# Kernel optimization log

Measured on AMD Instinct MI355X. Metric: run time of the kernel, lower is better.

The kernel has to match this reference:

```python
import jax, jax.numpy as jnp
import numpy as np

NUM_HEADS = 12
NUM_LANDMARKS = 64
EPS_REG = 1e-4


def setup_inputs() -> dict:
    key = jax.random.key(0)
    k1, k2, k3 = jax.random.split(key, 3)
    B, N, C = 4, 4096, 768
    x = jax.random.normal(k1, (B, N, C), dtype=jnp.float32)
    w_qkv = jax.random.normal(k2, (3 * C, C), dtype=jnp.float32) * (C ** -0.5)
    w_proj = jax.random.normal(k3, (C, C), dtype=jnp.float32) * (C ** -0.5)
    b_proj = jnp.zeros((C,), dtype=jnp.float32)
    return {"x": x, "w_qkv": w_qkv, "w_proj": w_proj, "b_proj": b_proj}


def _landmark_pool(t, m):
    # t: [B, H, N, D]; assumes N % m == 0 (true for chosen shapes)
    B, H, N, D = t.shape
    seg = N // m
    return t.reshape(B, H, m, seg, D).mean(axis=3)


def reference(x, w_qkv, w_proj, b_proj):
    B, N, C = x.shape
    H = NUM_HEADS
    D = C // H
    m = min(NUM_LANDMARKS, N)
    scale = D ** -0.5

    qkv = x @ w_qkv.T                              # [B, N, 3C]
    qkv = qkv.reshape(B, N, 3, H, D).transpose(2, 0, 3, 1, 4)
    q, k, v = qkv[0], qkv[1], qkv[2]               # [B, H, N, D]

    q_lm = _landmark_pool(q, m)                    # [B, H, m, D]
    k_lm = _landmark_pool(k, m)                    # [B, H, m, D]

    attn_q_km = jax.nn.softmax(jnp.einsum('bhnd,bhmd->bhnm', q, k_lm) * scale, axis=-1)
    attn_qm_km = jax.nn.softmax(jnp.einsum('bhld,bhmd->bhlm', q_lm, k_lm) * scale, axis=-1)
    attn_qm_k = jax.nn.softmax(jnp.einsum('bhmd,bhnd->bhmn', q_lm, k) * scale, axis=-1)

    eye = jnp.eye(m, dtype=attn_qm_km.dtype)
    inv_mid = jnp.linalg.inv(attn_qm_km + EPS_REG * eye)   # [B, H, m, m]

    out = attn_q_km @ (inv_mid @ (attn_qm_k @ v))          # [B, H, N, D]
    out = out.transpose(0, 2, 1, 3).reshape(B, N, C)
    out = out @ w_proj.T + b_proj
    return out
```

## Files before the change

kernel.cpp:

```cpp
#include <hip/hip_runtime.h>

typedef unsigned short u16;
typedef __attribute__((ext_vector_type(8))) short bf16x8;
typedef __attribute__((ext_vector_type(8))) unsigned short u16x8;
typedef __attribute__((ext_vector_type(4))) unsigned short u16x4;
typedef __attribute__((ext_vector_type(4))) float f32x4;

#define NB 4
#define NH 12
#define NSEQ 4096
#define NC 768
#define ND 64
#define NM 64
#define NBH 48

__device__ __forceinline__ float b2f(u16 u){ unsigned v = ((unsigned)u)<<16; return __builtin_bit_cast(float, v); }
__device__ __forceinline__ u16 f2b(float f){ unsigned u = __builtin_bit_cast(unsigned, f); u = u + 0x7FFFu + ((u>>16)&1u); return (u16)(u>>16); }
__device__ __forceinline__ void split2(float f, u16& h, u16& l){
  h = f2b(f);
  l = f2b(f - b2f(h));
}

typedef const __attribute__((address_space(1))) unsigned int guint;
typedef __attribute__((address_space(3))) unsigned int luint;
__device__ __forceinline__ void gload16(const void* g, void* l){
  __builtin_amdgcn_global_load_lds((guint*)g, (luint*)l, 16, 0, 0);
}

__device__ __forceinline__ f32x4 mfma16x16(bf16x8 a, bf16x8 b, f32x4 c){
  return __builtin_amdgcn_mfma_f32_16x16x32_bf16(a, b, c, 0, 0, 0);
}

#define NX4 3145728
#define NWQ4 442368
#define NWP4 147456
__global__ __launch_bounds__(256) void k_split3(const float* __restrict__ x, const float* __restrict__ wq,
                                                const float* __restrict__ wp,
                                                u16* __restrict__ xh, u16* __restrict__ xl,
                                                u16* __restrict__ wqh, u16* __restrict__ wql,
                                                u16* __restrict__ wph, u16* __restrict__ wpl){
  int i = blockIdx.x*256 + threadIdx.x;
  const float* src; u16 *dh, *dl; int j;
  if (i < NX4){ src = x; dh = xh; dl = xl; j = i; }
  else if (i < NX4+NWQ4){ src = wq; dh = wqh; dl = wql; j = i - NX4; }
  else if (i < NX4+NWQ4+NWP4){ src = wp; dh = wph; dl = wpl; j = i - NX4 - NWQ4; }
  else return;
  f32x4 v = ((const f32x4*)src)[j];
  u16x4 hh, ll;
  #pragma unroll
  for (int e=0;e<4;++e){ u16 hb, lb; split2(v[e], hb, lb); hh[e]=hb; ll[e]=lb; }
  ((u16x4*)dh)[j] = hh; ((u16x4*)dl)[j] = ll;
}


__global__ __launch_bounds__(256) void k_qkv(const u16* __restrict__ xh, const u16* __restrict__ xl,
                                             const u16* __restrict__ wh, const u16* __restrict__ wl,
                                             u16* __restrict__ qh, u16* __restrict__ ql,
                                             u16* __restrict__ kh, u16* __restrict__ kl,
                                             u16* __restrict__ vTh, u16* __restrict__ vTl,
                                             float* __restrict__ qlmf, float* __restrict__ klmf,
                                             u16* __restrict__ qlmh, u16* __restrict__ qlml,
                                             u16* __restrict__ klmh, u16* __restrict__ klml){
  __shared__ u16 lds[32768];
  const int K = NC;
  int tid = threadIdx.x, wave = tid>>6, lane = tid&63;
  int wm = wave>>1, wn = wave&1;
  int bid = blockIdx.x;
  int swz = (bid&7)*288 + (bid>>3);
  int bx = swz % 18, by = swz / 18;
  int m0 = by*128, n0 = bx*128;
  int srow = lane>>3;
  int scol = ((lane&7) ^ srow)*8;
  const u16* src0; u16* dst0;
  if (wave==0){ src0 = xh + (size_t)m0*K; dst0 = lds; }
  else if (wave==1){ src0 = xl + (size_t)m0*K; dst0 = lds+8192; }
  else if (wave==2){ src0 = wh + (size_t)n0*K; dst0 = lds+16384; }
  else            { src0 = wl + (size_t)n0*K; dst0 = lds+24576; }
  f32x4 acc[4][4] = {};
  for (int k0=0; k0<K; k0+=64){
    #pragma unroll
    for (int it=0; it<16; ++it){
      int r = it*8;
      gload16(&src0[(size_t)(r+srow)*K + k0 + scol], &dst0[r*64]);
    }
    __syncthreads();
    #pragma unroll
    for (int kk=0; kk<2; ++kk){
      int sl = ((kk*4 + (lane>>4)) ^ (lane&7))*8;
      bf16x8 a_h[4], a_l[4], b_h[4], b_l[4];
      #pragma unroll
      for (int i=0;i<4;++i){
        int ro = (wm*64+i*16+(lane&15))*64 + sl;
        a_h[i] = *(const bf16x8*)&lds[ro]; a_l[i] = *(const bf16x8*)&lds[8192+ro];
      }
      #pragma unroll
      for (int j=0;j<4;++j){
        int ro = (wn*64+j*16+(lane&15))*64 + sl;
        b_h[j] = *(const bf16x8*)&lds[16384+ro]; b_l[j] = *(const bf16x8*)&lds[24576+ro];
      }
      #pragma unroll
      for (int i=0;i<4;++i)
        #pragma unroll
        for (int j=0;j<4;++j){
          acc[i][j] = mfma16x16(a_h[i], b_h[j], acc[i][j]);
          acc[i][j] = mfma16x16(a_h[i], b_l[j], acc[i][j]);
          acc[i][j] = mfma16x16(a_l[i], b_h[j], acc[i][j]);
        }
    }
    __syncthreads();
  }
  int rb = (lane>>4)*4, cb = lane&15;
  int b_ = m0>>12, nlo = m0&4095;
  if (n0 < 1536){
    int s = n0/768;
    u16* dh = s ? kh : qh;
    u16* dl = s ? kl : ql;
    float* lmf = s ? klmf : qlmf;
    u16* lmh = s ? klmh : qlmh;
    u16* lml = s ? klml : qlml;
    #pragma unroll
    for (int j=0;j<4;++j){
      int gn = n0 + wn*64 + j*16 + cb;
      int rem = gn - s*768; int hd = rem>>6, d = rem&63;
      #pragma unroll
      for (int i=0;i<4;++i)
        #pragma unroll
        for (int r=0;r<4;++r){
          int n = nlo + wm*64 + i*16 + rb + r;
          size_t idx = (((size_t)(b_*NH + hd))*NSEQ + n)*ND + d;
          u16 hb, lb; split2(acc[i][j][r], hb, lb);
          dh[idx] = hb; dl[idx] = lb;
        }
      float tot = 0.f;
      #pragma unroll
      for (int i=0;i<4;++i)
        #pragma unroll
        for (int r=0;r<4;++r) tot += acc[i][j][r];
      tot += __shfl_xor(tot, 16);
      tot += __shfl_xor(tot, 32);
      if (lane < 16){
        int lseg = (nlo>>6) + wm;
        float mean = tot * (1.f/64.f);
        size_t o = (((size_t)(b_*NH + hd))*NM + lseg)*ND + d;
        lmf[o] = mean;
        u16 hb, lb; split2(mean, hb, lb);
        lmh[o] = hb; lml[o] = lb;
      }
    }
  } else {
    const int TS = 136;
    #pragma unroll
    for (int part=0; part<2; ++part){
      __syncthreads();
      #pragma unroll
      for (int j=0;j<4;++j){
        int dcol = wn*64 + j*16 + cb;
        #pragma unroll
        for (int i=0;i<4;++i)
          #pragma unroll
          for (int r=0;r<4;++r){
            int nrow = wm*64 + i*16 + rb + r;
            u16 hb, lb; split2(acc[i][j][r], hb, lb);
            lds[dcol*TS + nrow] = part ? lb : hb;
          }
      }
      __syncthreads();
      int drow = tid>>1, half = (tid&1)*64;
      int remd = (n0 - 1536) + drow;
      int hd = remd>>6, dd = remd&63;
      u16* dst = (part ? vTl : vTh) + (((size_t)(b_*NH + hd))*ND + dd)*NSEQ + nlo + half;
      const u16* srcl = &lds[drow*TS + half];
      #pragma unroll
      for (int e=0;e<8;++e)
        *(u16x8*)(dst + e*8) = *(const u16x8*)(srcl + e*8);
    }
  }
}

__global__ __launch_bounds__(256) void k_proj(const u16* __restrict__ Hh, const u16* __restrict__ Hl,
                                              const u16* __restrict__ wh, const u16* __restrict__ wl,
                                              const float* __restrict__ bias, float* __restrict__ out){
  __shared__ u16 lds[32768];
  const int K = NC;
  int tid = threadIdx.x, wave = tid>>6, lane = tid&63;
  int wm = wave>>1, wn = wave&1;
  int bid = blockIdx.x;
  int swz = (bid&7)*96 + (bid>>3);
  int bx = swz % 6, by = swz / 6;
  int m0 = by*128, n0 = bx*128;
  int srow = lane>>3;
  int scol = ((lane&7) ^ srow)*8;
  const u16* src0; u16* dst0;
  if (wave==0){ src0 = Hh + (size_t)m0*K; dst0 = lds; }
  else if (wave==1){ src0 = Hl + (size_t)m0*K; dst0 = lds+8192; }
  else if (wave==2){ src0 = wh + (size_t)n0*K; dst0 = lds+16384; }
  else            { src0 = wl + (size_t)n0*K; dst0 = lds+24576; }
  f32x4 acc[4][4] = {};
  for (int k0=0; k0<K; k0+=64){
    #pragma unroll
    for (int it=0; it<16; ++it){
      int r = it*8;
      gload16(&src0[(size_t)(r+srow)*K + k0 + scol], &dst0[r*64]);
    }
    __syncthreads();
    #pragma unroll
    for (int kk=0; kk<2; ++kk){
      int sl = ((kk*4 + (lane>>4)) ^ (lane&7))*8;
      bf16x8 a_h[4], a_l[4], b_h[4], b_l[4];
      #pragma unroll
      for (int i=0;i<4;++i){
        int ro = (wm*64+i*16+(lane&15))*64 + sl;
        a_h[i] = *(const bf16x8*)&lds[ro]; a_l[i] = *(const bf16x8*)&lds[8192+ro];
      }
      #pragma unroll
      for (int j=0;j<4;++j){
        int ro = (wn*64+j*16+(lane&15))*64 + sl;
        b_h[j] = *(const bf16x8*)&lds[16384+ro]; b_l[j] = *(const bf16x8*)&lds[24576+ro];
      }
      #pragma unroll
      for (int i=0;i<4;++i)
        #pragma unroll
        for (int j=0;j<4;++j){
          acc[i][j] = mfma16x16(a_h[i], b_h[j], acc[i][j]);
          acc[i][j] = mfma16x16(a_h[i], b_l[j], acc[i][j]);
          acc[i][j] = mfma16x16(a_l[i], b_h[j], acc[i][j]);
        }
    }
    __syncthreads();
  }
  int rb = (lane>>4)*4, cb = lane&15;
  #pragma unroll
  for (int j=0;j<4;++j){
    int gn = n0 + wn*64 + j*16 + cb;
    float bb = bias[gn];
    #pragma unroll
    for (int i=0;i<4;++i){
      #pragma unroll
      for (int r=0;r<4;++r){
        int gm = m0 + wm*64 + i*16 + rb + r;
        out[(size_t)gm*NC + gn] = acc[i][j][r] + bb;
      }
    }
  }
}

__global__ __launch_bounds__(256) void k_s2(const u16* __restrict__ qlmh, const u16* __restrict__ qlml,
                                            const u16* __restrict__ kh, const u16* __restrict__ kl,
                                            float* __restrict__ s2f){
  int chunk = blockIdx.x, bh = blockIdx.y;
  int tid = threadIdx.x, wave = tid>>6, lane = tid&63;
  const u16* Ahp = qlmh + (size_t)bh*NM*ND;
  const u16* Alp = qlml + (size_t)bh*NM*ND;
  const u16* Bhp = kh + (size_t)bh*NSEQ*ND;
  const u16* Blp = kl + (size_t)bh*NSEQ*ND;
  int nbase = chunk*256 + wave*64;
  f32x4 acc[4][4] = {};
  #pragma unroll
  for (int kk=0; kk<2; ++kk){
    int koff = kk*32 + (lane>>4)*8;
    bf16x8 a_h[4], a_l[4], b_h[4], b_l[4];
    #pragma unroll
    for (int i=0;i<4;++i){
      size_t ro = (size_t)(i*16+(lane&15))*ND + koff;
      a_h[i] = *(const bf16x8*)&Ahp[ro]; a_l[i] = *(const bf16x8*)&Alp[ro];
    }
    #pragma unroll
    for (int j=0;j<4;++j){
      size_t ro = (size_t)(nbase + j*16 + (lane&15))*ND + koff;
      b_h[j] = *(const bf16x8*)&Bhp[ro]; b_l[j] = *(const bf16x8*)&Blp[ro];
    }
    #pragma unroll
    for (int i=0;i<4;++i)
      #pragma unroll
      for (int j=0;j<4;++j){
        acc[i][j] = mfma16x16(a_h[i], b_h[j], acc[i][j]);
        acc[i][j] = mfma16x16(a_h[i], b_l[j], acc[i][j]);
        acc[i][j] = mfma16x16(a_l[i], b_h[j], acc[i][j]);
      }
  }
  int rb = (lane>>4)*4, cb = lane&15;
  #pragma unroll
  for (int i=0;i<4;++i)
    #pragma unroll
    for (int j=0;j<4;++j)
      #pragma unroll
      for (int r=0;r<4;++r){
        int l = i*16 + rb + r; int n = nbase + j*16 + cb;
        s2f[((size_t)bh*NM + l)*NSEQ + n] = acc[i][j][r]*0.125f;
      }
}

__global__ __launch_bounds__(256) void k_sm(float* __restrict__ s2region){
  int row = blockIdx.x;
  int tid = threadIdx.x, lane = tid&63, wid = tid>>6;
  __shared__ float redm[4], reds[4];
  const float* src = s2region + (size_t)row*NSEQ;
  const f32x4* ps = (const f32x4*)(src + (size_t)tid*16);
  f32x4 v0 = ps[0], v1 = ps[1], v2 = ps[2], v3 = ps[3];
  float vals[16];
  #pragma unroll
  for (int e=0;e<4;++e){ vals[e]=v0[e]; vals[4+e]=v1[e]; vals[8+e]=v2[e]; vals[12+e]=v3[e]; }
  float mx = -1e30f;
  #pragma unroll
  for (int j=0;j<16;++j) mx = fmaxf(mx, vals[j]);
  for (int off=32; off; off>>=1) mx = fmaxf(mx, __shfl_xor(mx, off));
  if (lane==0) redm[wid] = mx;
  __syncthreads();
  mx = fmaxf(fmaxf(redm[0],redm[1]), fmaxf(redm[2],redm[3]));
  float s = 0.f;
  #pragma unroll
  for (int j=0;j<16;++j){ vals[j] = __expf(vals[j]-mx); s += vals[j]; }
  for (int off=32; off; off>>=1) s += __shfl_xor(s, off);
  if (lane==0) reds[wid] = s;
  __syncthreads();
  s = reds[0]+reds[1]+reds[2]+reds[3];
  float inv = 1.f/s;
  u16* rh = (u16*)s2region + (size_t)row*8192;
  u16* rl = rh + 4096;
  u16x8 oh0, oh1, ol0, ol1;
  #pragma unroll
  for (int j=0;j<8;++j){
    u16 hb, lb;
    split2(vals[j]*inv, hb, lb);   oh0[j]=hb; ol0[j]=lb;
    split2(vals[8+j]*inv, hb, lb); oh1[j]=hb; ol1[j]=lb;
  }
  ((u16x8*)(rh + (size_t)tid*16))[0] = oh0;
  ((u16x8*)(rh + (size_t)tid*16))[1] = oh1;
  ((u16x8*)(rl + (size_t)tid*16))[0] = ol0;
  ((u16x8*)(rl + (size_t)tid*16))[1] = ol1;
}

__global__ __launch_bounds__(256) void k_t1(const u16* __restrict__ p2base, const u16* __restrict__ vTh,
                                            const u16* __restrict__ vTl, float* __restrict__ t1p){
  int kb = blockIdx.x, bh = blockIdx.y;
  int tid = threadIdx.x, wave = tid>>6, lane = tid&63;
  int arow = wave*16 + (lane&15);
  const u16* rowp = p2base + (size_t)(bh*64 + arow)*8192;
  const u16* Bh = vTh + (size_t)bh*ND*NSEQ;
  const u16* Bl = vTl + (size_t)bh*ND*NSEQ;
  f32x4 acc[4] = {};
  for (int ks=0; ks<16; ++ks){
    int koff = kb*512 + ks*32 + (lane>>4)*8;
    bf16x8 a_h = *(const bf16x8*)&rowp[koff];
    bf16x8 a_l = *(const bf16x8*)&rowp[4096 + koff];
    #pragma unroll
    for (int j=0;j<4;++j){
      size_t ro = (size_t)(j*16+(lane&15))*NSEQ + koff;
      bf16x8 b_h = *(const bf16x8*)&Bh[ro];
      bf16x8 b_l = *(const bf16x8*)&Bl[ro];
      acc[j] = mfma16x16(a_h, b_h, acc[j]);
      acc[j] = mfma16x16(a_h, b_l, acc[j]);
      acc[j] = mfma16x16(a_l, b_h, acc[j]);
    }
  }
  int rb = (lane>>4)*4, cb = lane&15;
  #pragma unroll
  for (int j=0;j<4;++j)
    #pragma unroll
    for (int r=0;r<4;++r){
      int l = wave*16 + rb + r; int d = j*16 + cb;
      t1p[((size_t)(kb*NBH + bh)*NM + l)*ND + d] = acc[j][r];
    }
}

__global__ __launch_bounds__(256) void k_mid(const float* __restrict__ qlmf, const float* __restrict__ klmf,
                                            const float* __restrict__ t1p,
                                            u16* __restrict__ w2th, u16* __restrict__ w2tl){
  __shared__ float M[64*68];
  __shared__ float T[64*68];
  __shared__ int piv_s;
  int bh = blockIdx.x, tid = threadIdx.x;
  int r = tid>>2, qd = tid&3;
  const float* qrow  = qlmf + (size_t)bh*NM*ND + r*64;
  const float* kbase = klmf + (size_t)bh*NM*ND;
  float qv[64];
  #pragma unroll
  for (int e=0;e<16;++e){
    f32x4 t4 = ((const f32x4*)qrow)[e];
    qv[e*4]=t4[0]; qv[e*4+1]=t4[1]; qv[e*4+2]=t4[2]; qv[e*4+3]=t4[3];
  }
  float sv[16];
  #pragma unroll
  for (int mi=0;mi<16;++mi){
    const float* krow = kbase + (size_t)(qd*16+mi)*64;
    float a = 0.f;
    #pragma unroll
    for (int e=0;e<16;++e){
      f32x4 k4 = ((const f32x4*)krow)[e];
      a += qv[e*4]*k4[0] + qv[e*4+1]*k4[1] + qv[e*4+2]*k4[2] + qv[e*4+3]*k4[3];
    }
    sv[mi] = a*0.125f;
  }
  float mx = sv[0];
  #pragma unroll
  for (int mi=1;mi<16;++mi) mx = fmaxf(mx, sv[mi]);
  mx = fmaxf(mx, __shfl_xor(mx,1)); mx = fmaxf(mx, __shfl_xor(mx,2));
  float sum = 0.f;
  #pragma unroll
  for (int mi=0;mi<16;++mi){ sv[mi] = __expf(sv[mi]-mx); sum += sv[mi]; }
  sum += __shfl_xor(sum,1); sum += __shfl_xor(sum,2);
  float sinv = 1.f/sum;
  #pragma unroll
  for (int mi=0;mi<16;++mi){
    int m = qd*16+mi;
    float p = sv[mi]*sinv;
    if (m == r) p += 1e-4f;
    M[r*68+m] = p;
  }
  #pragma unroll
  for (int q=0;q<4;++q){
    int c = qd*16 + q*4;
    f32x4 a = {};
    #pragma unroll
    for (int kb=0;kb<8;++kb)
      a += *(const f32x4*)&t1p[((size_t)(kb*NBH + bh)*NM + r)*ND + c];
    *(f32x4*)&T[r*68+c] = a;
  }
  __syncthreads();
  for (int kp=0; kp<64; ++kp){
    if (tid < 64){
      float val = (tid >= kp) ? fabsf(M[tid*68+kp]) : -1.f;
      int idx = tid;
      #pragma unroll
      for (int off=32; off; off>>=1){
        float ov = __shfl_xor(val, off); int oi = __shfl_xor(idx, off);
        if (ov > val || (ov == val && oi < idx)){ val = ov; idx = oi; }
      }
      if (tid == 0) piv_s = idx;
    }
    __syncthreads();
    int p = piv_s;
    if (r == kp){
      float pinv = 1.f / M[p*68+kp];
      f32x4 mk[4], mp[4], tk[4], tp_[4];
      #pragma unroll
      for (int q=0;q<4;++q){
        int c = qd*16 + q*4;
        mk[q] = *(const f32x4*)&M[kp*68+c]; mp[q] = *(const f32x4*)&M[p*68+c];
        tk[q] = *(const f32x4*)&T[kp*68+c]; tp_[q] = *(const f32x4*)&T[p*68+c];
      }
      #pragma unroll
      for (int q=0;q<4;++q){
        int c = qd*16 + q*4;
        *(f32x4*)&M[p*68+c] = mk[q];       *(f32x4*)&T[p*68+c] = tk[q];
        *(f32x4*)&M[kp*68+c] = mp[q]*pinv; *(f32x4*)&T[kp*68+c] = tp_[q]*pinv;
      }
    }
    __syncthreads();
    if (r != kp){
      float f = M[r*68+kp];
      #pragma unroll
      for (int q=0;q<4;++q){
        int c = qd*16 + q*4;
        f32x4 pm = *(const f32x4*)&M[kp*68+c];
        f32x4 om = *(const f32x4*)&M[r*68+c];
        *(f32x4*)&M[r*68+c] = om - f*pm;
        f32x4 pt = *(const f32x4*)&T[kp*68+c];
        f32x4 ot = *(const f32x4*)&T[r*68+c];
        *(f32x4*)&T[r*68+c] = ot - f*pt;
      }
    }
    __syncthreads();
  }
  int d = tid>>2, qs = tid&3;
  #pragma unroll
  for (int li=0; li<16; ++li){
    int l = qs*16 + li;
    float xv = T[l*68 + d];
    u16 hb, lb; split2(xv, hb, lb);
    size_t o = ((size_t)bh*ND + d)*NM + l;
    w2th[o] = hb; w2tl[o] = lb;
  }
}

__global__ __launch_bounds__(256) void k_final(const u16* __restrict__ qh, const u16* __restrict__ ql,
                                               const u16* __restrict__ klmh, const u16* __restrict__ klml,
                                               const u16* __restrict__ w2th, const u16* __restrict__ w2tl,
                                               u16* __restrict__ Hh, u16* __restrict__ Hl){
  __shared__ u16 Ph[4*4096], Pl[4*4096];
  int chunk = blockIdx.x, bh = blockIdx.y;
  int b_ = bh/NH, hd = bh - b_*NH;
  int tid = threadIdx.x, wave = tid>>6, lane = tid&63;
  int n0 = chunk*256 + wave*64;
  const u16* qhp = qh + ((size_t)bh*NSEQ + n0)*ND;
  const u16* qlp = ql + ((size_t)bh*NSEQ + n0)*ND;
  const u16* Kh = klmh + (size_t)bh*NM*ND;
  const u16* Kl = klml + (size_t)bh*NM*ND;
  const u16* Wh = w2th + (size_t)bh*ND*NM;
  const u16* Wl = w2tl + (size_t)bh*ND*NM;
  u16* Phw = Ph + wave*4096;
  u16* Plw = Pl + wave*4096;
  f32x4 accs[4][4] = {};
  #pragma unroll
  for (int kk=0; kk<2; ++kk){
    int koff = kk*32 + (lane>>4)*8;
    bf16x8 a_h[4], a_l[4], b_h[4], b_l[4];
    #pragma unroll
    for (int i=0;i<4;++i){
      size_t ro = (size_t)(i*16+(lane&15))*ND + koff;
      a_h[i] = *(const bf16x8*)&qhp[ro]; a_l[i] = *(const bf16x8*)&qlp[ro];
    }
    #pragma unroll
    for (int j=0;j<4;++j){
      size_t ro = (size_t)(j*16+(lane&15))*ND + koff;
      b_h[j] = *(const bf16x8*)&Kh[ro]; b_l[j] = *(const bf16x8*)&Kl[ro];
    }
    #pragma unroll
    for (int i=0;i<4;++i)
      #pragma unroll
      for (int j=0;j<4;++j){
        accs[i][j] = mfma16x16(a_h[i], b_h[j], accs[i][j]);
        accs[i][j] = mfma16x16(a_h[i], b_l[j], accs[i][j]);
        accs[i][j] = mfma16x16(a_l[i], b_h[j], accs[i][j]);
      }
  }
  #pragma unroll
  for (int i=0;i<4;++i)
    #pragma unroll
    for (int j=0;j<4;++j) accs[i][j] *= 0.125f;
  int rb = (lane>>4)*4, cb = lane&15;
  #pragma unroll
  for (int i=0;i<4;++i){
    #pragma unroll
    for (int r=0;r<4;++r){
      float mx = -1e30f;
      #pragma unroll
      for (int j=0;j<4;++j) mx = fmaxf(mx, accs[i][j][r]);
      #pragma unroll
      for (int off=1; off<16; off<<=1) mx = fmaxf(mx, __shfl_xor(mx, off));
      float e[4]; float sum = 0.f;
      #pragma unroll
      for (int j=0;j<4;++j){ e[j] = __expf(accs[i][j][r]-mx); sum += e[j]; }
      #pragma unroll
      for (int off=1; off<16; off<<=1) sum += __shfl_xor(sum, off);
      float inv = 1.f/sum;
      int row = i*16 + rb + r;
      #pragma unroll
      for (int j=0;j<4;++j){
        u16 hb, lb; split2(e[j]*inv, hb, lb);
        int col = j*16 + cb;
        int scol = (((col>>3) ^ (row&7))<<3) | (col&7);
        Phw[row*64 + scol] = hb;
        Plw[row*64 + scol] = lb;
      }
    }
  }
  __syncthreads();
  f32x4 acco[4][4] = {};
  #pragma unroll
  for (int kk=0; kk<2; ++kk){
    int koff = kk*32 + (lane>>4)*8;
    int sl = ((kk*4 + (lane>>4)) ^ (lane&7))*8;
    bf16x8 a_h[4], a_l[4], b_h[4], b_l[4];
    #pragma unroll
    for (int i=0;i<4;++i){
      int ro = (i*16+(lane&15))*64 + sl;
      a_h[i] = *(const bf16x8*)&Phw[ro]; a_l[i] = *(const bf16x8*)&Plw[ro];
    }
    #pragma unroll
    for (int j=0;j<4;++j){
      size_t ro = (size_t)(j*16+(lane&15))*64 + koff;
      b_h[j] = *(const bf16x8*)&Wh[ro]; b_l[j] = *(const bf16x8*)&Wl[ro];
    }
    #pragma unroll
    for (int i=0;i<4;++i)
      #pragma unroll
      for (int j=0;j<4;++j){
        acco[i][j] = mfma16x16(a_h[i], b_h[j], acco[i][j]);
        acco[i][j] = mfma16x16(a_h[i], b_l[j], acco[i][j]);
        acco[i][j] = mfma16x16(a_l[i], b_h[j], acco[i][j]);
      }
  }
  #pragma unroll
  for (int i=0;i<4;++i)
    #pragma unroll
    for (int j=0;j<4;++j)
      #pragma unroll
      for (int r=0;r<4;++r){
        int n = n0 + i*16 + rb + r;
        int d = j*16 + cb;
        size_t o = ((size_t)(b_*NSEQ + n))*NC + hd*64 + d;
        u16 hb, lb; split2(acco[i][j][r], hb, lb);
        Hh[o] = hb; Hl[o] = lb;
      }
}

__global__ void k_sent(float* out){ out[0] = 1.0e9f; }

#define OFF_QH     0ull
#define OFF_QL     25165824ull
#define OFF_KH     50331648ull
#define OFF_KL     75497472ull
#define OFF_VTH    100663296ull
#define OFF_VTL    125829120ull
#define OFF_S2     150994944ull
#define OFF_QLMF   201326592ull
#define OFF_KLMF   202113024ull
#define OFF_QLMH   202899456ull
#define OFF_QLML   203292672ull
#define OFF_KLMH   203685888ull
#define OFF_KLML   204079104ull
#define OFF_W2TH   204472320ull
#define OFF_W2TL   204865536ull
#define OFF_T1P    205258752ull
#define OFF_WQH    211550208ull
#define OFF_WQL    215089152ull
#define OFF_WPH    218628096ull
#define OFF_WPL    219807744ull
#define WS_NEEDED  220987392ull

extern "C" void kernel_launch(void* const* d_in, const int* in_sizes, int n_in,
                              void* d_out, int out_size, void* d_ws, size_t ws_size,
                              hipStream_t stream){
  const float* x     = (const float*)d_in[0];
  const float* wqkv  = (const float*)d_in[1];
  const float* wproj = (const float*)d_in[2];
  const float* bproj = (const float*)d_in[3];
  float* out = (float*)d_out;
  char* ws = (char*)d_ws;
  if (ws_size < WS_NEEDED){ k_sent<<<1,1,0,stream>>>(out); return; }
  u16* qh = (u16*)(ws + OFF_QH);  u16* ql = (u16*)(ws + OFF_QL);
  u16* kh = (u16*)(ws + OFF_KH);  u16* kl = (u16*)(ws + OFF_KL);
  u16* vTh = (u16*)(ws + OFF_VTH); u16* vTl = (u16*)(ws + OFF_VTL);
  u16* xh = (u16*)(ws + OFF_S2);
  u16* xl = (u16*)(ws + OFF_S2 + 25165824ull);
  float* s2f = (float*)(ws + OFF_S2);
  u16* p2base = (u16*)(ws + OFF_S2);
  u16* Hh = (u16*)(ws + OFF_S2);
  u16* Hl = (u16*)(ws + OFF_S2 + 25165824ull);
  float* qlmf = (float*)(ws + OFF_QLMF);
  float* klmf = (float*)(ws + OFF_KLMF);
  u16* qlmh = (u16*)(ws + OFF_QLMH); u16* qlml = (u16*)(ws + OFF_QLML);
  u16* klmh = (u16*)(ws + OFF_KLMH); u16* klml = (u16*)(ws + OFF_KLML);
  u16* w2th = (u16*)(ws + OFF_W2TH); u16* w2tl = (u16*)(ws + OFF_W2TL);
  float* t1p = (float*)(ws + OFF_T1P);
  u16* wqh = (u16*)(ws + OFF_WQH); u16* wql = (u16*)(ws + OFF_WQL);
  u16* wph = (u16*)(ws + OFF_WPH); u16* wpl = (u16*)(ws + OFF_WPL);

  k_split3   <<<14592, 256, 0, stream>>>(x, wqkv, wproj, xh, xl, wqh, wql, wph, wpl);
  k_qkv      <<<2304, 256, 0, stream>>>(xh, xl, wqh, wql, qh, ql, kh, kl, vTh, vTl,
                                        qlmf, klmf, qlmh, qlml, klmh, klml);
  k_s2       <<<dim3(16,48),  256, 0, stream>>>(qlmh, qlml, kh, kl, s2f);
  k_sm       <<<3072,         256, 0, stream>>>(s2f);
  k_t1       <<<dim3(8,48),   256, 0, stream>>>(p2base, vTh, vTl, t1p);
  k_mid      <<<48,           256, 0, stream>>>(qlmf, klmf, t1p, w2th, w2tl);
  k_final    <<<dim3(16,48),  256, 0, stream>>>(qh, ql, klmh, klml, w2th, w2tl, Hh, Hl);
  k_proj     <<<768,          256, 0, stream>>>(Hh, Hl, wph, wpl, bproj, out);
}
```

Measured before the change: 499.4 us.

## Fuse row softmax into score and T1 kernels via partial max/sum stats

Removes the standalone k_sm softmax pass. k_s2 now emits per-chunk, per-wave row max and exp-sum partials, and k_t1 combines them into a global max and normalizer, then applies exp, scaling and the bf16 hi/lo split on the fly while loading scores. This saves one kernel launch and a full read/write pass over the 48x64x4096 score matrix. In exchange k_t1 reads fp32 scores (twice the bytes of the old bf16 pair), recomputes exp for every element, and reduces 64 stat entries per row. The stats buffer reuses the wq weight workspace region, which is dead after k_qkv.

Measured after the change: 495.3 us (median of 2 runs). About the same (-0.8%).

```diff
diff --git a/kernel.cpp b/kernel.cpp
--- a/kernel.cpp
+++ b/kernel.cpp
@@ -246,7 +246,7 @@
 
 __global__ __launch_bounds__(256) void k_s2(const u16* __restrict__ qlmh, const u16* __restrict__ qlml,
                                             const u16* __restrict__ kh, const u16* __restrict__ kl,
-                                            float* __restrict__ s2f){
+                                            float* __restrict__ s2f, float* __restrict__ stats){
   int chunk = blockIdx.x, bh = blockIdx.y;
   int tid = threadIdx.x, wave = tid>>6, lane = tid&63;
   const u16* Ahp = qlmh + (size_t)bh*NM*ND;
@@ -288,61 +288,60 @@
         int l = i*16 + rb + r; int n = nbase + j*16 + cb;
         s2f[((size_t)bh*NM + l)*NSEQ + n] = acc[i][j][r]*0.125f;
       }
-}
-
-__global__ __launch_bounds__(256) void k_sm(float* __restrict__ s2region){
-  int row = blockIdx.x;
-  int tid = threadIdx.x, lane = tid&63, wid = tid>>6;
-  __shared__ float redm[4], reds[4];
-  const float* src = s2region + (size_t)row*NSEQ;
-  const f32x4* ps = (const f32x4*)(src + (size_t)tid*16);
-  f32x4 v0 = ps[0], v1 = ps[1], v2 = ps[2], v3 = ps[3];
-  float vals[16];
-  #pragma unroll
-  for (int e=0;e<4;++e){ vals[e]=v0[e]; vals[4+e]=v1[e]; vals[8+e]=v2[e]; vals[12+e]=v3[e]; }
-  float mx = -1e30f;
-  #pragma unroll
-  for (int j=0;j<16;++j) mx = fmaxf(mx, vals[j]);
-  for (int off=32; off; off>>=1) mx = fmaxf(mx, __shfl_xor(mx, off));
-  if (lane==0) redm[wid] = mx;
-  __syncthreads();
-  mx = fmaxf(fmaxf(redm[0],redm[1]), fmaxf(redm[2],redm[3]));
-  float s = 0.f;
-  #pragma unroll
-  for (int j=0;j<16;++j){ vals[j] = __expf(vals[j]-mx); s += vals[j]; }
-  for (int off=32; off; off>>=1) s += __shfl_xor(s, off);
-  if (lane==0) reds[wid] = s;
-  __syncthreads();
-  s = reds[0]+reds[1]+reds[2]+reds[3];
-  float inv = 1.f/s;
-  u16* rh = (u16*)s2region + (size_t)row*8192;
-  u16* rl = rh + 4096;
-  u16x8 oh0, oh1, ol0, ol1;
-  #pragma unroll
-  for (int j=0;j<8;++j){
-    u16 hb, lb;
-    split2(vals[j]*inv, hb, lb);   oh0[j]=hb; ol0[j]=lb;
-    split2(vals[8+j]*inv, hb, lb); oh1[j]=hb; ol1[j]=lb;
-  }
-  ((u16x8*)(rh + (size_t)tid*16))[0] = oh0;
-  ((u16x8*)(rh + (size_t)tid*16))[1] = oh1;
-  ((u16x8*)(rl + (size_t)tid*16))[0] = ol0;
-  ((u16x8*)(rl + (size_t)tid*16))[1] = ol1;
-}
-
-__global__ __launch_bounds__(256) void k_t1(const u16* __restrict__ p2base, const u16* __restrict__ vTh,
-                                            const u16* __restrict__ vTl, float* __restrict__ t1p){
+  #pragma unroll
+  for (int i=0;i<4;++i)
+    #pragma unroll
+    for (int r=0;r<4;++r){
+      float v0 = acc[i][0][r]*0.125f, v1 = acc[i][1][r]*0.125f;
+      float v2 = acc[i][2][r]*0.125f, v3 = acc[i][3][r]*0.125f;
+      float mx = fmaxf(fmaxf(v0,v1), fmaxf(v2,v3));
+      #pragma unroll
+      for (int off=1; off<16; off<<=1) mx = fmaxf(mx, __shfl_xor(mx, off));
+      float se = __expf(v0-mx)+__expf(v1-mx)+__expf(v2-mx)+__expf(v3-mx);
+      #pragma unroll
+      for (int off=1; off<16; off<<=1) se += __shfl_xor(se, off);
+      if (cb == 0){
+        int row = i*16 + rb + r;
+        size_t o = ((((size_t)chunk*NBH + bh)*4 + wave)*64 + row)*2;
+        stats[o] = mx; stats[o+1] = se;
+      }
+    }
+}
+
+__global__ __launch_bounds__(256) void k_t1(const float* __restrict__ s2f, const float* __restrict__ stats,
+                                            const u16* __restrict__ vTh, const u16* __restrict__ vTl,
+                                            float* __restrict__ t1p){
   int kb = blockIdx.x, bh = blockIdx.y;
   int tid = threadIdx.x, wave = tid>>6, lane = tid&63;
   int arow = wave*16 + (lane&15);
-  const u16* rowp = p2base + (size_t)(bh*64 + arow)*8192;
+  float MX = -1e30f;
+  for (int c=0;c<16;++c)
+    #pragma unroll
+    for (int w=0;w<4;++w)
+      MX = fmaxf(MX, stats[((((size_t)c*NBH + bh)*4 + w)*64 + arow)*2]);
+  float SE = 0.f;
+  for (int c=0;c<16;++c)
+    #pragma unroll
+    for (int w=0;w<4;++w){
+      size_t o = ((((size_t)c*NBH + bh)*4 + w)*64 + arow)*2;
+      SE += stats[o+1]*__expf(stats[o]-MX);
+    }
+  float INV = 1.f/SE;
+  const float* srow = s2f + ((size_t)bh*NM + arow)*NSEQ;
   const u16* Bh = vTh + (size_t)bh*ND*NSEQ;
   const u16* Bl = vTl + (size_t)bh*ND*NSEQ;
   f32x4 acc[4] = {};
   for (int ks=0; ks<16; ++ks){
     int koff = kb*512 + ks*32 + (lane>>4)*8;
-    bf16x8 a_h = *(const bf16x8*)&rowp[koff];
-    bf16x8 a_l = *(const bf16x8*)&rowp[4096 + koff];
+    f32x4 sv0 = *(const f32x4*)&srow[koff];
+    f32x4 sv1 = *(const f32x4*)&srow[koff+4];
+    bf16x8 a_h, a_l;
+    #pragma unroll
+    for (int e=0;e<4;++e){
+      u16 hb, lb;
+      split2(__expf(sv0[e]-MX)*INV, hb, lb); a_h[e]   = (short)hb; a_l[e]   = (short)lb;
+      split2(__expf(sv1[e]-MX)*INV, hb, lb); a_h[4+e] = (short)hb; a_l[4+e] = (short)lb;
+    }
     #pragma unroll
     for (int j=0;j<4;++j){
       size_t ro = (size_t)(j*16+(lane&15))*NSEQ + koff;
@@ -625,7 +624,6 @@
   u16* xh = (u16*)(ws + OFF_S2);
   u16* xl = (u16*)(ws + OFF_S2 + 25165824ull);
   float* s2f = (float*)(ws + OFF_S2);
-  u16* p2base = (u16*)(ws + OFF_S2);
   u16* Hh = (u16*)(ws + OFF_S2);
   u16* Hl = (u16*)(ws + OFF_S2 + 25165824ull);
   float* qlmf = (float*)(ws + OFF_QLMF);
@@ -636,13 +634,13 @@
   float* t1p = (float*)(ws + OFF_T1P);
   u16* wqh = (u16*)(ws + OFF_WQH); u16* wql = (u16*)(ws + OFF_WQL);
   u16* wph = (u16*)(ws + OFF_WPH); u16* wpl = (u16*)(ws + OFF_WPL);
+  float* stats = (float*)(ws + OFF_WQH);
 
   k_split3   <<<14592, 256, 0, stream>>>(x, wqkv, wproj, xh, xl, wqh, wql, wph, wpl);
   k_qkv      <<<2304, 256, 0, stream>>>(xh, xl, wqh, wql, qh, ql, kh, kl, vTh, vTl,
                                         qlmf, klmf, qlmh, qlml, klmh, klml);
-  k_s2       <<<dim3(16,48),  256, 0, stream>>>(qlmh, qlml, kh, kl, s2f);
-  k_sm       <<<3072,         256, 0, stream>>>(s2f);
-  k_t1       <<<dim3(8,48),   256, 0, stream>>>(p2base, vTh, vTl, t1p);
+  k_s2       <<<dim3(16,48),  256, 0, stream>>>(qlmh, qlml, kh, kl, s2f, stats);
+  k_t1       <<<dim3(8,48),   256, 0, stream>>>(s2f, stats, vTh, vTl, t1p);
   k_mid      <<<48,           256, 0, stream>>>(qlmf, klmf, t1p, w2th, w2tl);
   k_final    <<<dim3(16,48),  256, 0, stream>>>(qh, ql, klmh, klml, w2th, w2tl, Hh, Hl);
   k_proj     <<<768,          256, 0, stream>>>(Hh, Hl, wph, wpl, bproj, out);
```
